# Kernel optimization log

Measured on AMD Instinct MI355X. Metric: run time of the kernel, lower is better.

Reference implementation:

```python
import jax, jax.numpy as jnp
import numpy as np

B, N, U = 16, 1024, 64  # batch, nodes, num_units
ALPHA = 0.2  # LeakyReLU negative slope
NEG = -9e15


def setup_inputs() -> dict:
    key = jax.random.key(0)
    ks = jax.random.split(key, 7)
    X = jax.random.normal(ks[0], (B, N, U), dtype=jnp.float32)
    state = jax.random.normal(ks[1], (B, N, U), dtype=jnp.float32)
    # random sparse adjacency (avg degree ~32) with self-loops
    adj = (jax.random.uniform(ks[2], (N, N)) < 32.0 / N).astype(jnp.float32)
    adj = jnp.maximum(adj, jnp.eye(N, dtype=jnp.float32))
    def xavier(k, shape):
        fan_in, fan_out = shape
        s = 1.414 * np.sqrt(6.0 / (fan_in + fan_out))
        return jax.random.uniform(k, shape, jnp.float32, -s, s)
    W1 = xavier(ks[3], (2 * U, 2 * U))   # gat_1: in 2U -> out 2U
    a1 = xavier(ks[4], (4 * U, 1))       # attention vector, 2*out
    W2 = xavier(ks[5], (2 * U, U))       # gat_2: in 2U -> out U
    a2 = xavier(ks[6], (2 * U, 1))
    return {"X": X, "state": state, "adj": adj, "W1": W1, "a1": a1, "W2": W2, "a2": a2}


def _gat_layer(x, adj, W, a):
    # x: [b,n,f_in], W: [f_in,F], a: [2F,1]
    h = jnp.einsum('bnf,fo->bno', x, W)              # [b,n,F]
    F_out = W.shape[1]
    s_src = h @ a[:F_out, 0]                         # [b,n] contribution of node i
    s_dst = h @ a[F_out:, 0]                         # [b,n] contribution of node j
    e = jax.nn.leaky_relu(s_src[:, :, None] + s_dst[:, None, :], ALPHA)  # [b,n,n]
    e = jnp.where(adj[None, :, :] > 0, e, NEG)
    att = jax.nn.softmax(e, axis=2)                  # masked softmax over neighbors j
    return jnp.einsum('bij,bjf->bif', att, h)        # [b,n,F]


def reference(X, state, adj, W1, a1, W2, a2):
    X1 = jnp.concatenate([X, state], axis=2)         # [b,n,2U]
    gv = jax.nn.sigmoid(_gat_layer(X1, adj, W1, a1)) # [b,n,2U]
    r, z = jnp.split(gv, 2, axis=2)                  # each [b,n,U]
    X2 = jnp.concatenate([X, r * state], axis=2)
    h_t1 = jnp.tanh(_gat_layer(X2, adj, W2, a2))     # [b,n,U]
    new_h = z * state + (1.0 - z) * h_t1
    return new_h
```

## Files before the change

kernel.cpp:

```cpp
#include <hip/hip_runtime.h>

#define BB 16
#define NN 1024
#define LALPHA 0.2f
#define MAXD 192

__global__ void build_csr(const float* __restrict__ adj, int* __restrict__ deg,
                          int* __restrict__ cols) {
    __shared__ int cnt;
    int i = blockIdx.x;
    if (threadIdx.x == 0) cnt = 0;
    __syncthreads();
    for (int j = threadIdx.x; j < NN; j += blockDim.x) {
        if (adj[(size_t)i * NN + j] > 0.0f) {
            int p = atomicAdd(&cnt, 1);
            if (p < MAXD) cols[(size_t)i * MAXD + p] = j;
        }
    }
    __syncthreads();
    if (threadIdx.x == 0) deg[i] = cnt < MAXD ? cnt : MAXD;
}

template <int FOUT, int RB>
__global__ void gemm_score(const float* __restrict__ A0, const float* __restrict__ A1,
                           const float* __restrict__ W, const float* __restrict__ avec,
                           float* __restrict__ h, float* __restrict__ s_src,
                           float* __restrict__ s_dst) {
    constexpr int TFN = FOUT / 4;
    constexpr int NT = (RB / 4) * TFN;
    __shared__ float xs[RB][132];
    int t = threadIdx.x;
    int tf = t % TFN, tr = t / TFN;
    int f0 = tf * 4, r0 = tr * 4;
    int base = blockIdx.x * RB;

    for (int idx = t; idx < RB * 32; idx += NT) {
        int r = idx >> 5, c = (idx & 31) * 4;
        float4 v = (c < 64) ? *(const float4*)(A0 + (size_t)(base + r) * 64 + c)
                            : *(const float4*)(A1 + (size_t)(base + r) * 64 + (c - 64));
        xs[r][c] = v.x; xs[r][c + 1] = v.y; xs[r][c + 2] = v.z; xs[r][c + 3] = v.w;
    }
    __syncthreads();

    float acc[4][4] = {};
    for (int k = 0; k < 128; k += 4) {
        float4 xv[4], wv[4];
#pragma unroll
        for (int i = 0; i < 4; i++) xv[i] = *(const float4*)&xs[r0 + i][k];
#pragma unroll
        for (int i = 0; i < 4; i++) wv[i] = *(const float4*)(W + (size_t)(k + i) * FOUT + f0);
#pragma unroll
        for (int i = 0; i < 4; i++) {
            float xr[4] = {xv[i].x, xv[i].y, xv[i].z, xv[i].w};
#pragma unroll
            for (int kk = 0; kk < 4; kk++) {
                acc[i][0] += xr[kk] * wv[kk].x;
                acc[i][1] += xr[kk] * wv[kk].y;
                acc[i][2] += xr[kk] * wv[kk].z;
                acc[i][3] += xr[kk] * wv[kk].w;
            }
        }
    }

    float a_s[4], a_d[4];
#pragma unroll
    for (int i = 0; i < 4; i++) {
        a_s[i] = avec[f0 + i];
        a_d[i] = avec[FOUT + f0 + i];
    }
#pragma unroll
    for (int i = 0; i < 4; i++) {
        int m = base + r0 + i;
        *(float4*)(h + (size_t)m * FOUT + f0) =
            make_float4(acc[i][0], acc[i][1], acc[i][2], acc[i][3]);
        float ps = acc[i][0] * a_s[0] + acc[i][1] * a_s[1] + acc[i][2] * a_s[2] + acc[i][3] * a_s[3];
        float pd = acc[i][0] * a_d[0] + acc[i][1] * a_d[1] + acc[i][2] * a_d[2] + acc[i][3] * a_d[3];
#pragma unroll
        for (int o = TFN / 2; o >= 1; o >>= 1) {
            ps += __shfl_xor(ps, o);
            pd += __shfl_xor(pd, o);
        }
        if (tf == 0) {
            s_src[m] = ps;
            s_dst[m] = pd;
        }
    }
}

__global__ void attn1_kernel(const int* __restrict__ deg, const int* __restrict__ cols,
                             const float* __restrict__ h1, const float* __restrict__ s_src,
                             const float* __restrict__ s_dst, const float* __restrict__ state,
                             float* __restrict__ rstate, float* __restrict__ zbuf) {
    int bi = blockIdx.x;
    int i = bi & (NN - 1);
    int b = bi >> 10;
    int lane = threadIdx.x;
    int d = deg[i];
    float ssrc = s_src[bi];
    __shared__ float w[MAXD];
    __shared__ int cl[MAXD];
    for (int j = lane; j < d; j += 64) cl[j] = cols[(size_t)i * MAXD + j];
    __syncthreads();
    float mx = -1e30f;
    for (int j = lane; j < d; j += 64) {
        float e = ssrc + s_dst[b * NN + cl[j]];
        e = e > 0.f ? e : LALPHA * e;
        w[j] = e;
        mx = fmaxf(mx, e);
    }
#pragma unroll
    for (int o = 32; o >= 1; o >>= 1) mx = fmaxf(mx, __shfl_xor(mx, o));
    float sum = 0.f;
    for (int j = lane; j < d; j += 64) {
        float e = __expf(w[j] - mx);
        w[j] = e;
        sum += e;
    }
#pragma unroll
    for (int o = 32; o >= 1; o >>= 1) sum += __shfl_xor(sum, o);
    __syncthreads();
    float inv = 1.f / sum;
    float acc0 = 0.f, acc1 = 0.f;
    int j = 0;
    for (; j + 1 < d; j += 2) {
        float w0 = w[j], w1 = w[j + 1];
        const float* p0 = h1 + (size_t)(b * NN + cl[j]) * 128;
        const float* p1 = h1 + (size_t)(b * NN + cl[j + 1]) * 128;
        float x0 = p0[lane], y0 = p0[lane + 64];
        float x1 = p1[lane], y1 = p1[lane + 64];
        acc0 += w0 * x0 + w1 * x1;
        acc1 += w0 * y0 + w1 * y1;
    }
    if (j < d) {
        float w0 = w[j];
        const float* p0 = h1 + (size_t)(b * NN + cl[j]) * 128;
        acc0 += w0 * p0[lane];
        acc1 += w0 * p0[lane + 64];
    }
    float rg = 1.f / (1.f + __expf(-acc0 * inv));
    float zg = 1.f / (1.f + __expf(-acc1 * inv));
    float st = state[(size_t)bi * 64 + lane];
    rstate[(size_t)bi * 64 + lane] = rg * st;
    zbuf[(size_t)bi * 64 + lane] = zg;
}

__global__ void attn2_kernel(const int* __restrict__ deg, const int* __restrict__ cols,
                             const float* __restrict__ h2, const float* __restrict__ s_src,
                             const float* __restrict__ s_dst, const float* __restrict__ state,
                             const float* __restrict__ zbuf, float* __restrict__ out) {
    int bi = blockIdx.x;
    int i = bi & (NN - 1);
    int b = bi >> 10;
    int lane = threadIdx.x;
    int d = deg[i];
    float ssrc = s_src[bi];
    __shared__ float w[MAXD];
    __shared__ int cl[MAXD];
    for (int j = lane; j < d; j += 64) cl[j] = cols[(size_t)i * MAXD + j];
    __syncthreads();
    float mx = -1e30f;
    for (int j = lane; j < d; j += 64) {
        float e = ssrc + s_dst[b * NN + cl[j]];
        e = e > 0.f ? e : LALPHA * e;
        w[j] = e;
        mx = fmaxf(mx, e);
    }
#pragma unroll
    for (int o = 32; o >= 1; o >>= 1) mx = fmaxf(mx, __shfl_xor(mx, o));
    float sum = 0.f;
    for (int j = lane; j < d; j += 64) {
        float e = __expf(w[j] - mx);
        w[j] = e;
        sum += e;
    }
#pragma unroll
    for (int o = 32; o >= 1; o >>= 1) sum += __shfl_xor(sum, o);
    __syncthreads();
    float inv = 1.f / sum;
    float acc = 0.f;
    int j = 0;
    for (; j + 1 < d; j += 2) {
        float w0 = w[j], w1 = w[j + 1];
        const float* p0 = h2 + (size_t)(b * NN + cl[j]) * 64;
        const float* p1 = h2 + (size_t)(b * NN + cl[j + 1]) * 64;
        acc += w0 * p0[lane] + w1 * p1[lane];
    }
    if (j < d) acc += w[j] * h2[(size_t)(b * NN + cl[j]) * 64 + lane];
    float ht = tanhf(acc * inv);
    float z = zbuf[(size_t)bi * 64 + lane];
    float st = state[(size_t)bi * 64 + lane];
    out[(size_t)bi * 64 + lane] = z * st + (1.f - z) * ht;
}

extern "C" void kernel_launch(void* const* d_in, const int* in_sizes, int n_in,
                              void* d_out, int out_size, void* d_ws, size_t ws_size,
                              hipStream_t stream) {
    const float* X     = (const float*)d_in[0];
    const float* state = (const float*)d_in[1];
    const float* adj   = (const float*)d_in[2];
    const float* W1    = (const float*)d_in[3];
    const float* a1    = (const float*)d_in[4];
    const float* W2    = (const float*)d_in[5];
    const float* a2    = (const float*)d_in[6];
    float* out = (float*)d_out;

    char* ws = (char*)d_ws;
    size_t off = 0;
    auto alloc = [&](size_t bytes) -> void* {
        void* p = ws + off;
        off = (off + bytes + 255) & ~(size_t)255;
        return p;
    };
    int*   deg    = (int*)alloc(NN * sizeof(int));
    int*   cols   = (int*)alloc((size_t)NN * MAXD * sizeof(int));
    float* h1     = (float*)alloc((size_t)BB * NN * 128 * sizeof(float));
    float* ssrc1  = (float*)alloc((size_t)BB * NN * sizeof(float));
    float* sdst1  = (float*)alloc((size_t)BB * NN * sizeof(float));
    float* rstate = (float*)alloc((size_t)BB * NN * 64 * sizeof(float));
    float* zbuf   = (float*)alloc((size_t)BB * NN * 64 * sizeof(float));
    float* h2     = (float*)alloc((size_t)BB * NN * 64 * sizeof(float));
    float* ssrc2  = (float*)alloc((size_t)BB * NN * sizeof(float));
    float* sdst2  = (float*)alloc((size_t)BB * NN * sizeof(float));

    const int M = BB * NN;

    build_csr<<<NN, 256, 0, stream>>>(adj, deg, cols);
    gemm_score<128, 32><<<M / 32, 256, 0, stream>>>(X, state, W1, a1, h1, ssrc1, sdst1);
    attn1_kernel<<<M, 64, 0, stream>>>(deg, cols, h1, ssrc1, sdst1, state, rstate, zbuf);
    gemm_score<64, 64><<<M / 64, 256, 0, stream>>>(X, rstate, W2, a2, h2, ssrc2, sdst2);
    attn2_kernel<<<M, 64, 0, stream>>>(deg, cols, h2, ssrc2, sdst2, state, zbuf, out);
}
```

Baseline: 141.9 us.

## Split each node's attention aggregation across two waves in 256-thread blocks

Both attention kernels now launch 256-thread blocks that handle two nodes, with two 64-lane waves per node. In attn1 each wave aggregates one 64-feature half of h1; in attn2 the two waves take alternate neighbors and combine their partial sums through shared memory. Attention logits stay in registers and the column and score loads are fused into one pass, with no block barriers before aggregation. The aim is more waves in flight to hide the latency of the gather loads, at the cost of each wave of a node recomputing the same softmax and relying on wave-local ordering of shared-memory accesses.

```diff
diff --git a/kernel.cpp b/kernel.cpp
--- a/kernel.cpp
+++ b/kernel.cpp
@@ -87,109 +87,132 @@
     }
 }
 
-__global__ void attn1_kernel(const int* __restrict__ deg, const int* __restrict__ cols,
-                             const float* __restrict__ h1, const float* __restrict__ s_src,
-                             const float* __restrict__ s_dst, const float* __restrict__ state,
-                             float* __restrict__ rstate, float* __restrict__ zbuf) {
-    int bi = blockIdx.x;
+__global__ __launch_bounds__(256) void attn1_kernel(
+    const int* __restrict__ deg, const int* __restrict__ cols,
+    const float* __restrict__ h1, const float* __restrict__ s_src,
+    const float* __restrict__ s_dst, const float* __restrict__ state,
+    float* __restrict__ rstate, float* __restrict__ zbuf) {
+    int wv = threadIdx.x >> 6;
+    int lane = threadIdx.x & 63;
+    int node = wv >> 1;
+    int half = wv & 1;
+    int bi = blockIdx.x * 2 + node;
     int i = bi & (NN - 1);
     int b = bi >> 10;
-    int lane = threadIdx.x;
     int d = deg[i];
     float ssrc = s_src[bi];
-    __shared__ float w[MAXD];
-    __shared__ int cl[MAXD];
-    for (int j = lane; j < d; j += 64) cl[j] = cols[(size_t)i * MAXD + j];
-    __syncthreads();
+    __shared__ float w[2][MAXD];
+    __shared__ int cl[2][MAXD];
+
+    float ev[3];
     float mx = -1e30f;
-    for (int j = lane; j < d; j += 64) {
-        float e = ssrc + s_dst[b * NN + cl[j]];
+    int nslot = 0;
+    for (int j = lane; j < d; j += 64, nslot++) {
+        int c = cols[(size_t)i * MAXD + j];
+        cl[node][j] = c;
+        float e = ssrc + s_dst[b * NN + c];
         e = e > 0.f ? e : LALPHA * e;
-        w[j] = e;
+        ev[nslot] = e;
         mx = fmaxf(mx, e);
     }
 #pragma unroll
     for (int o = 32; o >= 1; o >>= 1) mx = fmaxf(mx, __shfl_xor(mx, o));
     float sum = 0.f;
-    for (int j = lane; j < d; j += 64) {
-        float e = __expf(w[j] - mx);
-        w[j] = e;
-        sum += e;
+    {
+        int s = 0;
+        for (int j = lane; j < d; j += 64, s++) {
+            float p = __expf(ev[s] - mx);
+            sum += p;
+            w[node][j] = p;
+        }
     }
 #pragma unroll
     for (int o = 32; o >= 1; o >>= 1) sum += __shfl_xor(sum, o);
-    __syncthreads();
     float inv = 1.f / sum;
-    float acc0 = 0.f, acc1 = 0.f;
-    int j = 0;
-    for (; j + 1 < d; j += 2) {
-        float w0 = w[j], w1 = w[j + 1];
-        const float* p0 = h1 + (size_t)(b * NN + cl[j]) * 128;
-        const float* p1 = h1 + (size_t)(b * NN + cl[j + 1]) * 128;
-        float x0 = p0[lane], y0 = p0[lane + 64];
-        float x1 = p1[lane], y1 = p1[lane + 64];
-        acc0 += w0 * x0 + w1 * x1;
-        acc1 += w0 * y0 + w1 * y1;
-    }
-    if (j < d) {
-        float w0 = w[j];
-        const float* p0 = h1 + (size_t)(b * NN + cl[j]) * 128;
-        acc0 += w0 * p0[lane];
-        acc1 += w0 * p0[lane + 64];
-    }
-    float rg = 1.f / (1.f + __expf(-acc0 * inv));
-    float zg = 1.f / (1.f + __expf(-acc1 * inv));
-    float st = state[(size_t)bi * 64 + lane];
-    rstate[(size_t)bi * 64 + lane] = rg * st;
-    zbuf[(size_t)bi * 64 + lane] = zg;
-}
-
-__global__ void attn2_kernel(const int* __restrict__ deg, const int* __restrict__ cols,
-                             const float* __restrict__ h2, const float* __restrict__ s_src,
-                             const float* __restrict__ s_dst, const float* __restrict__ state,
-                             const float* __restrict__ zbuf, float* __restrict__ out) {
-    int bi = blockIdx.x;
-    int i = bi & (NN - 1);
-    int b = bi >> 10;
-    int lane = threadIdx.x;
-    int d = deg[i];
-    float ssrc = s_src[bi];
-    __shared__ float w[MAXD];
-    __shared__ int cl[MAXD];
-    for (int j = lane; j < d; j += 64) cl[j] = cols[(size_t)i * MAXD + j];
-    __syncthreads();
-    float mx = -1e30f;
-    for (int j = lane; j < d; j += 64) {
-        float e = ssrc + s_dst[b * NN + cl[j]];
-        e = e > 0.f ? e : LALPHA * e;
-        w[j] = e;
-        mx = fmaxf(mx, e);
-    }
-#pragma unroll
-    for (int o = 32; o >= 1; o >>= 1) mx = fmaxf(mx, __shfl_xor(mx, o));
-    float sum = 0.f;
-    for (int j = lane; j < d; j += 64) {
-        float e = __expf(w[j] - mx);
-        w[j] = e;
-        sum += e;
-    }
-#pragma unroll
-    for (int o = 32; o >= 1; o >>= 1) sum += __shfl_xor(sum, o);
-    __syncthreads();
-    float inv = 1.f / sum;
+
+    const float* hb = h1 + (size_t)b * NN * 128 + half * 64;
     float acc = 0.f;
     int j = 0;
     for (; j + 1 < d; j += 2) {
-        float w0 = w[j], w1 = w[j + 1];
-        const float* p0 = h2 + (size_t)(b * NN + cl[j]) * 64;
-        const float* p1 = h2 + (size_t)(b * NN + cl[j + 1]) * 64;
+        float w0 = w[node][j], w1 = w[node][j + 1];
+        const float* p0 = hb + (size_t)cl[node][j] * 128;
+        const float* p1 = hb + (size_t)cl[node][j + 1] * 128;
         acc += w0 * p0[lane] + w1 * p1[lane];
     }
-    if (j < d) acc += w[j] * h2[(size_t)(b * NN + cl[j]) * 64 + lane];
-    float ht = tanhf(acc * inv);
-    float z = zbuf[(size_t)bi * 64 + lane];
+    if (j < d) acc += w[node][j] * (hb + (size_t)cl[node][j] * 128)[lane];
+
+    float g = 1.f / (1.f + __expf(-acc * inv));
     float st = state[(size_t)bi * 64 + lane];
-    out[(size_t)bi * 64 + lane] = z * st + (1.f - z) * ht;
+    if (half == 0)
+        rstate[(size_t)bi * 64 + lane] = g * st;
+    else
+        zbuf[(size_t)bi * 64 + lane] = g;
+}
+
+__global__ __launch_bounds__(256) void attn2_kernel(
+    const int* __restrict__ deg, const int* __restrict__ cols,
+    const float* __restrict__ h2, const float* __restrict__ s_src,
+    const float* __restrict__ s_dst, const float* __restrict__ state,
+    const float* __restrict__ zbuf, float* __restrict__ out) {
+    int wv = threadIdx.x >> 6;
+    int lane = threadIdx.x & 63;
+    int node = wv >> 1;
+    int half = wv & 1;
+    int bi = blockIdx.x * 2 + node;
+    int i = bi & (NN - 1);
+    int b = bi >> 10;
+    int d = deg[i];
+    float ssrc = s_src[bi];
+    __shared__ float w[2][MAXD];
+    __shared__ int cl[2][MAXD];
+    __shared__ float part[2][64];
+
+    float ev[3];
+    float mx = -1e30f;
+    int nslot = 0;
+    for (int j = lane; j < d; j += 64, nslot++) {
+        int c = cols[(size_t)i * MAXD + j];
+        cl[node][j] = c;
+        float e = ssrc + s_dst[b * NN + c];
+        e = e > 0.f ? e : LALPHA * e;
+        ev[nslot] = e;
+        mx = fmaxf(mx, e);
+    }
+#pragma unroll
+    for (int o = 32; o >= 1; o >>= 1) mx = fmaxf(mx, __shfl_xor(mx, o));
+    float sum = 0.f;
+    {
+        int s = 0;
+        for (int j = lane; j < d; j += 64, s++) {
+            float p = __expf(ev[s] - mx);
+            sum += p;
+            w[node][j] = p;
+        }
+    }
+#pragma unroll
+    for (int o = 32; o >= 1; o >>= 1) sum += __shfl_xor(sum, o);
+    float inv = 1.f / sum;
+
+    const float* hb = h2 + (size_t)b * NN * 64;
+    float acc = 0.f;
+    int j = half;
+    for (; j + 2 < d; j += 4) {
+        float w0 = w[node][j], w1 = w[node][j + 2];
+        const float* p0 = hb + (size_t)cl[node][j] * 64;
+        const float* p1 = hb + (size_t)cl[node][j + 2] * 64;
+        acc += w0 * p0[lane] + w1 * p1[lane];
+    }
+    for (; j < d; j += 2) acc += w[node][j] * (hb + (size_t)cl[node][j] * 64)[lane];
+
+    if (half == 1) part[node][lane] = acc;
+    __syncthreads();
+    if (half == 0) {
+        acc += part[node][lane];
+        float ht = tanhf(acc * inv);
+        float z = zbuf[(size_t)bi * 64 + lane];
+        float st = state[(size_t)bi * 64 + lane];
+        out[(size_t)bi * 64 + lane] = z * st + (1.f - z) * ht;
+    }
 }
 
 extern "C" void kernel_launch(void* const* d_in, const int* in_sizes, int n_in,
@@ -226,7 +249,7 @@
 
     build_csr<<<NN, 256, 0, stream>>>(adj, deg, cols);
     gemm_score<128, 32><<<M / 32, 256, 0, stream>>>(X, state, W1, a1, h1, ssrc1, sdst1);
-    attn1_kernel<<<M, 64, 0, stream>>>(deg, cols, h1, ssrc1, sdst1, state, rstate, zbuf);
+    attn1_kernel<<<M / 2, 256, 0, stream>>>(deg, cols, h1, ssrc1, sdst1, state, rstate, zbuf);
     gemm_score<64, 64><<<M / 64, 256, 0, stream>>>(X, rstate, W2, a2, h2, ssrc2, sdst2);
-    attn2_kernel<<<M, 64, 0, stream>>>(deg, cols, h2, ssrc2, sdst2, state, zbuf, out);
-}
+    attn2_kernel<<<M / 2, 256, 0, stream>>>(deg, cols, h2, ssrc2, sdst2, state, zbuf, out);
+}
```

Result: slower. 160.2 us (+12.9%).
